# Optimization experiments

Hardware: AMD Instinct MI355X
Metric: run time of the kernel (lower is better)

The kernel has to match this reference:

```python
import jax, jax.numpy as jnp
import numpy as np

N = 50000      # nodes
E = 1600000    # edges (avg degree 32)
F_IN = 128
HID = 256
C = 40


def setup_inputs() -> dict:
    key = jax.random.key(0)
    ks = jax.random.split(key, 12)
    x = jax.random.normal(ks[0], (N, F_IN), jnp.float32)
    edge_index = jax.random.randint(ks[1], (2, E), 0, N, dtype=jnp.int32)

    def glorot(k, fan_in, fan_out):
        s = jnp.sqrt(2.0 / (fan_in + fan_out)).astype(jnp.float32)
        return jax.random.normal(k, (fan_in, fan_out), jnp.float32) * s

    return {
        "x": x,
        "edge_index": edge_index,
        "W1": glorot(ks[2], F_IN, HID), "b1": jnp.zeros((HID,), jnp.float32),
        "W2": glorot(ks[3], HID, HID),  "b2": jnp.zeros((HID,), jnp.float32),
        "W3": glorot(ks[4], HID, HID),  "b3": jnp.zeros((HID,), jnp.float32),
        "W4": glorot(ks[5], HID, C),    "b4": jnp.zeros((C,), jnp.float32),
    }


def _gcn_conv(x, W, b, src, dst, norm_e, self_norm):
    # PyG GCNConv: h = X W; out_j = sum_i norm_ij * h_i  (+ self-loop term) + b
    h = x @ W                                   # [N, F_out]
    msg = h[src] * norm_e[:, None]              # [E, F_out] gather + scale
    agg = jax.ops.segment_sum(msg, dst, num_segments=N)
    agg = agg + h * self_norm[:, None]          # self-loop contribution
    return agg + b


def reference(x, edge_index, W1, b1, W2, b2, W3, b3, W4, b4):
    src, dst = edge_index[0], edge_index[1]
    # degree on A + I (self-loops added), computed over destination nodes
    deg = jax.ops.segment_sum(jnp.ones((E,), x.dtype), dst, num_segments=N) + 1.0
    inv_sqrt = jax.lax.rsqrt(deg)               # [N]
    norm_e = inv_sqrt[src] * inv_sqrt[dst]      # [E] symmetric norm per edge
    self_norm = inv_sqrt * inv_sqrt             # [N] self-loop norm = 1/deg

    h = jax.nn.relu(_gcn_conv(x, W1, b1, src, dst, norm_e, self_norm))
    h = jax.nn.relu(_gcn_conv(h, W2, b2, src, dst, norm_e, self_norm))
    h = jax.nn.relu(_gcn_conv(h, W3, b3, src, dst, norm_e, self_norm))
    h = _gcn_conv(h, W4, b4, src, dst, norm_e, self_norm)
    return jax.nn.log_softmax(h, axis=1)
```

## Files before the change

### kernel.cpp

```cpp
#include <hip/hip_runtime.h>
#include <hip/hip_fp16.h>
#include <math.h>


typedef _Float16 f16x8 __attribute__((ext_vector_type(8)));
typedef float f32x4 __attribute__((ext_vector_type(4)));
typedef unsigned u32x4 __attribute__((ext_vector_type(4)));

#define CAP 80

#define AS1 __attribute__((address_space(1)))
#define AS3 __attribute__((address_space(3)))

__device__ __forceinline__ void dma16(const unsigned short* g,
                                      const unsigned short* ldsBase) {
    __builtin_amdgcn_global_load_lds((const AS1 void*)(size_t)g,
                                     (AS3 void*)(unsigned)(size_t)ldsBase,
                                     16, 0, 0);
}

__device__ __forceinline__ __half2 u2h2(unsigned u) {
    union { unsigned u; __half2 h; } v; v.u = u; return v.h;
}
__device__ __forceinline__ unsigned h22u(__half2 h) {
    union { unsigned u; __half2 h; } v; v.h = h; return v.u;
}
__device__ __forceinline__ float hlo(unsigned u) {
    return __half2float(__ushort_as_half((unsigned short)(u & 0xFFFFu)));
}
__device__ __forceinline__ float hhi(unsigned u) {
    return __half2float(__ushort_as_half((unsigned short)(u >> 16)));
}

__global__ __launch_bounds__(256) void count_prep_kernel(
        const int* __restrict__ dst,
        int* __restrict__ cnt, int* __restrict__ rank, int E, int nEdgeBlocks,
        const float* __restrict__ x, unsigned short* __restrict__ xb, int nx4,
        const float* __restrict__ W1, const float* __restrict__ W2,
        const float* __restrict__ W3, const float* __restrict__ W4,
        unsigned short* __restrict__ Wt1, unsigned short* __restrict__ Wt2,
        unsigned short* __restrict__ Wt3, unsigned short* __restrict__ Wt4) {
    int b = blockIdx.x;
    if (b < nEdgeBlocks) {
        int e = b * 256 + threadIdx.x;
        if (e < E) rank[e] = atomicAdd(&cnt[dst[e]], 1);
        return;
    }
    int i = (b - nEdgeBlocks) * 256 + threadIdx.x;
    if (i < nx4) {
        float4 v = reinterpret_cast<const float4*>(x)[i];
        ushort4 o;
        o.x = __half_as_ushort(__float2half_rn(v.x));
        o.y = __half_as_ushort(__float2half_rn(v.y));
        o.z = __half_as_ushort(__float2half_rn(v.z));
        o.w = __half_as_ushort(__float2half_rn(v.w));
        reinterpret_cast<ushort4*>(xb)[i] = o;
        return;
    }
    int j = i - nx4;
    if (j < 32768) {
        int k = j >> 8, n = j & 255;
        Wt1[n * 128 + k] = __half_as_ushort(__float2half_rn(W1[j]));
    } else if (j < 98304) {
        int t = j - 32768; int k = t >> 8, n = t & 255;
        Wt2[n * 256 + k] = __half_as_ushort(__float2half_rn(W2[t]));
    } else if (j < 163840) {
        int t = j - 98304; int k = t >> 8, n = t & 255;
        Wt3[n * 256 + k] = __half_as_ushort(__float2half_rn(W3[t]));
    } else if (j < 174080) {
        int t = j - 163840; int k = t / 40, n = t - k * 40;
        Wt4[n * 256 + k] = __half_as_ushort(__float2half_rn(W4[t]));
    }
}

__global__ __launch_bounds__(256) void scatter_rsq_kernel(
        const int* __restrict__ src, const int* __restrict__ dst,
        const int* __restrict__ rank, unsigned short* __restrict__ epk,
        int E, int nEdgeBlocks,
        const int* __restrict__ cnt, float* __restrict__ rsq, int N) {
    int b = blockIdx.x;
    if (b < nEdgeBlocks) {
        int e = b * 256 + threadIdx.x;
        if (e < E) {
            int d = dst[e];
            int s = src[e];
            int r = rank[e]; if (r >= CAP) r = CAP - 1;
            epk[(size_t)d * CAP + r] = (unsigned short)s;
        }
        return;
    }
    int n = (b - nEdgeBlocks) * 256 + threadIdx.x;
    if (n < N) rsq[n] = rsqrtf((float)cnt[n] + 1.0f);
}

template <int ROWB, bool WSRC, bool BIAS, bool RELU>
__global__ __launch_bounds__(256) void agg_wide_kernel(
        const unsigned short* __restrict__ G,
        const int* __restrict__ cnt,
        const unsigned short* __restrict__ epk,
        const float* __restrict__ rsq,
        const float* __restrict__ bias,
        unsigned short* __restrict__ out, int N) {
    constexpr int ROWS = ROWB / 2;
    constexpr int LPN = ROWB / 16;
    constexpr int LOG_LPN = (LPN == 32) ? 5 : 4;
    constexpr int NPW = 64 / LPN;
    int lane = threadIdx.x & 63;
    int wid = threadIdx.x >> 6;
    int sub = lane >> LOG_LPN;
    int off = lane & (LPN - 1);
    int node = blockIdx.x * (4 * NPW) + wid * NPW + sub;
    if (node >= N) return;

    const unsigned short* gb = G + off * 8;
    const unsigned short* ep = epk + (size_t)node * CAP;
    int deg = cnt[node]; if (deg > CAP) deg = CAP;

    __half2 acc[4];
    #pragma unroll
    for (int k = 0; k < 4; k++) acc[k] = u2h2(0u);

    int e = 0;
    for (; e + 7 < deg; e += 8) {
        uint4 pv = *reinterpret_cast<const uint4*>(ep + e);
        int s[8];
        s[0] = pv.x & 0xFFFFu; s[1] = pv.x >> 16;
        s[2] = pv.y & 0xFFFFu; s[3] = pv.y >> 16;
        s[4] = pv.z & 0xFFFFu; s[5] = pv.z >> 16;
        s[6] = pv.w & 0xFFFFu; s[7] = pv.w >> 16;
        uint4 v[8];
        #pragma unroll
        for (int j = 0; j < 8; j++)
            v[j] = *reinterpret_cast<const uint4*>(gb + (size_t)s[j] * ROWS);
        if (WSRC) {
            float ws[8];
            #pragma unroll
            for (int j = 0; j < 8; j++) ws[j] = rsq[s[j]];
            #pragma unroll
            for (int j = 0; j < 8; j++) {
                __half2 w2 = __half2half2(__float2half_rn(ws[j]));
                acc[0] = __hfma2(w2, u2h2(v[j].x), acc[0]);
                acc[1] = __hfma2(w2, u2h2(v[j].y), acc[1]);
                acc[2] = __hfma2(w2, u2h2(v[j].z), acc[2]);
                acc[3] = __hfma2(w2, u2h2(v[j].w), acc[3]);
            }
        } else {
            #pragma unroll
            for (int j = 0; j < 8; j++) {
                acc[0] = __hadd2(acc[0], u2h2(v[j].x));
                acc[1] = __hadd2(acc[1], u2h2(v[j].y));
                acc[2] = __hadd2(acc[2], u2h2(v[j].z));
                acc[3] = __hadd2(acc[3], u2h2(v[j].w));
            }
        }
    }
    for (; e < deg; e++) {
        int s0 = ep[e];
        uint4 v0 = *reinterpret_cast<const uint4*>(gb + (size_t)s0 * ROWS);
        if (WSRC) {
            __half2 w2 = __half2half2(__float2half_rn(rsq[s0]));
            acc[0] = __hfma2(w2, u2h2(v0.x), acc[0]);
            acc[1] = __hfma2(w2, u2h2(v0.y), acc[1]);
            acc[2] = __hfma2(w2, u2h2(v0.z), acc[2]);
            acc[3] = __hfma2(w2, u2h2(v0.w), acc[3]);
        } else {
            acc[0] = __hadd2(acc[0], u2h2(v0.x));
            acc[1] = __hadd2(acc[1], u2h2(v0.y));
            acc[2] = __hadd2(acc[2], u2h2(v0.z));
            acc[3] = __hadd2(acc[3], u2h2(v0.w));
        }
    }

    float r = rsq[node];
    uint4 sv = *reinterpret_cast<const uint4*>(gb + (size_t)node * ROWS);
    unsigned svu[4] = {sv.x, sv.y, sv.z, sv.w};
    float sw = WSRC ? r : 1.0f;
    float r2 = r * r;
    u32x4 wp;
    float4 bv0, bv1;
    if (!WSRC && BIAS) {
        bv0 = reinterpret_cast<const float4*>(bias)[off * 2];
        bv1 = reinterpret_cast<const float4*>(bias)[off * 2 + 1];
    }
    float bvf[8] = {bv0.x, bv0.y, bv0.z, bv0.w, bv1.x, bv1.y, bv1.z, bv1.w};
    #pragma unroll
    for (int k = 0; k < 4; k++) {
        float2 f = __half22float2(acc[k]);
        f.x = fmaf(sw, hlo(svu[k]), f.x);
        f.y = fmaf(sw, hhi(svu[k]), f.y);
        float ox, oy;
        if (WSRC) {
            ox = r * f.x; oy = r * f.y;
        } else {
            ox = r2 * f.x; oy = r2 * f.y;
            if (BIAS) {
                ox = fmaf(r, bvf[2 * k], ox);
                oy = fmaf(r, bvf[2 * k + 1], oy);
            }
            if (RELU) { ox = fmaxf(ox, 0.f); oy = fmaxf(oy, 0.f); }
        }
        wp[k] = h22u(__floats2half2_rn(ox, oy));
    }
    __builtin_nontemporal_store(
        wp, reinterpret_cast<u32x4*>(out + (size_t)node * ROWS + off * 8));
}

__global__ __launch_bounds__(256) void agg40_softmax_kernel(
        const unsigned short* __restrict__ G,
        const int* __restrict__ cnt,
        const unsigned short* __restrict__ epk,
        const float* __restrict__ rsq,
        const float* __restrict__ bias,
        float* __restrict__ out, int N) {
    __shared__ __align__(16) unsigned red[4][64][4];
    int lane = threadIdx.x & 63;
    int wid = threadIdx.x >> 6;
    int node = blockIdx.x * 4 + wid;
    if (node >= N) return;
    const unsigned short* ep = epk + (size_t)node * CAP;
    int deg = cnt[node]; if (deg > CAP) deg = CAP;

    int j = lane / 5;
    int c = lane - j * 5;
    __half2 a0 = u2h2(0u), a1 = u2h2(0u), a2 = u2h2(0u), a3 = u2h2(0u);
    for (int e0 = 0; e0 < deg; e0 += 12) {
        int e = e0 + j;
        unsigned m = (j < 12 && e < deg) ? 0xFFFFFFFFu : 0u;
        int ee = (e < deg) ? e : (deg - 1);
        int s = ep[ee];
        u32x4 v = *reinterpret_cast<const u32x4*>(G + (size_t)s * 40 + c * 8);
        a0 = __hadd2(a0, u2h2(v.x & m));
        a1 = __hadd2(a1, u2h2(v.y & m));
        a2 = __hadd2(a2, u2h2(v.z & m));
        a3 = __hadd2(a3, u2h2(v.w & m));
    }
    u32x4 packed;
    packed.x = h22u(a0); packed.y = h22u(a1);
    packed.z = h22u(a2); packed.w = h22u(a3);
    *reinterpret_cast<u32x4*>(&red[wid][lane][0]) = packed;
    bool act = lane < 20;
    __half2 acch = u2h2(0u);
    if (act) {
        int cc = lane >> 2;
        int w = lane & 3;
        #pragma unroll
        for (int jj = 0; jj < 12; jj++)
            acch = __hadd2(acch, u2h2(red[wid][5 * jj + cc][w]));
    }
    float lo = 0.f, hi = 0.f;
    if (act) {
        float r = rsq[node];
        unsigned sv = reinterpret_cast<const unsigned*>(G)[(size_t)node * 20 + lane];
        float2 f = __half22float2(acch);
        f.x += hlo(sv); f.y += hhi(sv);
        lo = fmaf(r, f.x, bias[2 * lane]);
        hi = fmaf(r, f.y, bias[2 * lane + 1]);
    }
    float m = act ? fmaxf(lo, hi) : -INFINITY;
    #pragma unroll
    for (int o = 32; o >= 1; o >>= 1) m = fmaxf(m, __shfl_xor(m, o, 64));
    float s = act ? (expf(lo - m) + expf(hi - m)) : 0.f;
    #pragma unroll
    for (int o = 32; o >= 1; o >>= 1) s += __shfl_xor(s, o, 64);
    float ls = logf(s);
    if (act) {
        float2 o2;
        o2.x = lo - m - ls;
        o2.y = hi - m - ls;
        *reinterpret_cast<float2*>(out + (size_t)node * 40 + 2 * lane) = o2;
    }
}

template <int BK, bool BIAS, bool RELU, bool SCALE>
__global__ __launch_bounds__(256) void gemm_f16(
        const unsigned short* __restrict__ A,
        const unsigned short* __restrict__ Bt,
        const float* __restrict__ bias,
        const float* __restrict__ rsqRow,
        unsigned short* __restrict__ Cout,
        int M, int K, int Nc) {
    constexpr int SPR = BK / 8;
    constexpr int NSTG = (128 * SPR) / 256;
    __shared__ __align__(16) unsigned short As[128 * BK];
    __shared__ __align__(16) unsigned short Bs[128 * BK];
    int tid = threadIdx.x;
    int lane = tid & 63;
    int wid = tid >> 6;
    int rowBase = blockIdx.y * 128;
    int colBase = blockIdx.x * 128;
    int waveM = (wid & 1) * 64;
    int waveN = (wid >> 1) * 64;

    f32x4 acc[4][4] = {};
    int lrow = lane & 15;
    int kgrp = (lane >> 4) * 8;

    for (int k0 = 0; k0 < K; k0 += BK) {
        #pragma unroll
        for (int c = 0; c < NSTG; c++) {
            int base16 = c * 256 + wid * 64;
            int slot = base16 + lane;
            int row = slot / SPR;
            int kp = (slot % SPR) * 8;
            int ksw = kp ^ ((row & (SPR - 1)) * 8);
            int gr = rowBase + row; if (gr >= M) gr = M - 1;
            dma16(A + (size_t)gr * K + k0 + ksw, &As[base16 * 8]);
            int gc = colBase + row; if (gc >= Nc) gc = Nc - 1;
            dma16(Bt + (size_t)gc * K + k0 + ksw, &Bs[base16 * 8]);
        }
        __syncthreads();
        #pragma unroll
        for (int kk = 0; kk < BK; kk += 32) {
            f16x8 af[4], bfr[4];
            #pragma unroll
            for (int t = 0; t < 4; t++) {
                int ra = waveM + t * 16 + lrow;
                af[t] = *reinterpret_cast<const f16x8*>(
                    &As[ra * BK + ((kk + kgrp) ^ ((ra & (SPR - 1)) * 8))]);
                int rb = waveN + t * 16 + lrow;
                bfr[t] = *reinterpret_cast<const f16x8*>(
                    &Bs[rb * BK + ((kk + kgrp) ^ ((rb & (SPR - 1)) * 8))]);
            }
            #pragma unroll
            for (int mt = 0; mt < 4; mt++)
                #pragma unroll
                for (int nt = 0; nt < 4; nt++)
                    acc[mt][nt] = __builtin_amdgcn_mfma_f32_16x16x32_f16(
                        af[mt], bfr[nt], acc[mt][nt], 0, 0, 0);
        }
        __syncthreads();
    }

    #pragma unroll
    for (int mt = 0; mt < 4; mt++) {
        #pragma unroll
        for (int r = 0; r < 4; r++) {
            int row = rowBase + waveM + mt * 16 + (lane >> 4) * 4 + r;
            if (row >= M) continue;
            float rs = SCALE ? rsqRow[row] : 1.0f;
            #pragma unroll
            for (int nt = 0; nt < 4; nt++) {
                int col = colBase + waveN + nt * 16 + (lane & 15);
                if (col >= Nc) continue;
                float v = acc[mt][nt][r];
                if (BIAS) v += bias[col];
                if (RELU) v = fmaxf(v, 0.f);
                if (SCALE) v *= rs;
                Cout[(size_t)row * Nc + col] = __half_as_ushort(__float2half_rn(v));
            }
        }
    }
}


extern "C" void kernel_launch(void* const* d_in, const int* in_sizes, int n_in,
                              void* d_out, int out_size, void* d_ws, size_t ws_size,
                              hipStream_t stream) {
    const float* x  = (const float*)d_in[0];
    const int*   ei = (const int*)d_in[1];
    const float* W1 = (const float*)d_in[2];
    const float* b1 = (const float*)d_in[3];
    const float* W2 = (const float*)d_in[4];
    const float* b2 = (const float*)d_in[5];
    const float* W3 = (const float*)d_in[6];
    const float* b3 = (const float*)d_in[7];
    const float* W4 = (const float*)d_in[8];
    const float* b4 = (const float*)d_in[9];

    const int FIN = 128, HID = 256, C = 40;
    const int N = in_sizes[0] / FIN;
    const int E = in_sizes[1] / 2;
    const int* src = ei;
    const int* dst = ei + E;

    char* w = (char*)d_ws;
    auto alloc = [&](size_t bytes) {
        char* p = w;
        w += (bytes + 255) & ~(size_t)255;
        return p;
    };
    int*   cnt    = (int*)alloc((size_t)N * 4);
    float* rsq    = (float*)alloc((size_t)N * 4);
    unsigned short* epk = (unsigned short*)alloc((size_t)N * CAP * 2);
    unsigned short* aggx = (unsigned short*)alloc((size_t)N * FIN * 2);
    unsigned short* bufA = (unsigned short*)alloc((size_t)N * HID * 2);
    unsigned short* bufB = (unsigned short*)alloc((size_t)N * HID * 2);
    unsigned short* Wt1 = (unsigned short*)alloc((size_t)FIN * HID * 2);
    unsigned short* Wt2 = (unsigned short*)alloc((size_t)HID * HID * 2);
    unsigned short* Wt3 = (unsigned short*)alloc((size_t)HID * HID * 2);
    unsigned short* Wt4 = (unsigned short*)alloc((size_t)HID * C * 2);
    unsigned short* xb = bufB;
    int* rank = (int*)aggx;

    hipMemsetAsync(cnt, 0, (size_t)N * 4, stream);

    int nx4 = N * FIN / 4;
    int nEdgeBlocks = (E + 255) / 256;
    int prepBlocks = (nx4 + 174080 + 255) / 256;
    count_prep_kernel<<<nEdgeBlocks + prepBlocks, 256, 0, stream>>>(
        dst, cnt, rank, E, nEdgeBlocks,
        x, xb, nx4, W1, W2, W3, W4, Wt1, Wt2, Wt3, Wt4);
    int rsqBlocks = (N + 255) / 256;
    scatter_rsq_kernel<<<nEdgeBlocks + rsqBlocks, 256, 0, stream>>>(
        src, dst, rank, epk, E, nEdgeBlocks, cnt, rsq, N);

    dim3 gAgg1((N + 15) / 16);
    dim3 gAggH((N + 7) / 8);
    int grp = (N + 3) / 4;
    dim3 gHID((HID + 127) / 128, (N + 127) / 128);
    dim3 gC((C + 127) / 128, (N + 127) / 128);

    agg_wide_kernel<256, true, false, false>
        <<<gAgg1, 256, 0, stream>>>(xb, cnt, epk, rsq, nullptr, aggx, N);
    gemm_f16<128, true, true, true><<<gHID, 256, 0, stream>>>(
        aggx, Wt1, b1, rsq, bufA, N, FIN, HID);
    gemm_f16<128, false, false, false><<<gHID, 256, 0, stream>>>(
        bufA, Wt2, nullptr, nullptr, bufB, N, HID, HID);
    agg_wide_kernel<512, false, true, true>
        <<<gAggH, 256, 0, stream>>>(bufB, cnt, epk, rsq, b2, bufA, N);
    gemm_f16<128, false, false, false><<<gHID, 256, 0, stream>>>(
        bufA, Wt3, nullptr, nullptr, bufB, N, HID, HID);
    agg_wide_kernel<512, false, true, true>
        <<<gAggH, 256, 0, stream>>>(bufB, cnt, epk, rsq, b3, bufA, N);
    gemm_f16<128, false, false, false><<<gC, 256, 0, stream>>>(
        bufA, Wt4, nullptr, nullptr, bufB, N, HID, C);
    agg40_softmax_kernel<<<grp, 256, 0, stream>>>(bufB, cnt, epk,
                                                  rsq, b4, (float*)d_out, N);
}
```

Baseline: 562.6 us.

## Privatize degree counters into 8 slices and vectorize edge count/scatter

Degree counting now uses 8 private counter arrays chosen by block index, which cuts atomic contention on hot destinations. Each thread handles 4 edges through int4 loads. A new small kernel prefix-sums the 8 slices into per-slice base offsets, total counts and rsqrt norms, and the scatter adds the slice base to each edge's local rank. In exchange it adds an extra kernel launch, a larger memset and 8N-sized scratch buffers.

```diff
diff --git a/kernel.cpp b/kernel.cpp
--- a/kernel.cpp
+++ b/kernel.cpp
@@ -34,16 +34,29 @@
 
 __global__ __launch_bounds__(256) void count_prep_kernel(
         const int* __restrict__ dst,
-        int* __restrict__ cnt, int* __restrict__ rank, int E, int nEdgeBlocks,
+        int* __restrict__ cnt8, int* __restrict__ rank, int E, int nEdgeBlocks,
         const float* __restrict__ x, unsigned short* __restrict__ xb, int nx4,
+        int N,
         const float* __restrict__ W1, const float* __restrict__ W2,
         const float* __restrict__ W3, const float* __restrict__ W4,
         unsigned short* __restrict__ Wt1, unsigned short* __restrict__ Wt2,
         unsigned short* __restrict__ Wt3, unsigned short* __restrict__ Wt4) {
     int b = blockIdx.x;
     if (b < nEdgeBlocks) {
-        int e = b * 256 + threadIdx.x;
-        if (e < E) rank[e] = atomicAdd(&cnt[dst[e]], 1);
+        int* cs = cnt8 + (size_t)(b & 7) * N;
+        int e0 = b * 1024 + threadIdx.x * 4;
+        if (e0 + 3 < E) {
+            int4 d4 = *reinterpret_cast<const int4*>(dst + e0);
+            int4 r4;
+            r4.x = atomicAdd(&cs[d4.x], 1);
+            r4.y = atomicAdd(&cs[d4.y], 1);
+            r4.z = atomicAdd(&cs[d4.z], 1);
+            r4.w = atomicAdd(&cs[d4.w], 1);
+            *reinterpret_cast<int4*>(rank + e0) = r4;
+        } else {
+            for (int e = e0; e < E; e++)
+                rank[e] = atomicAdd(&cs[dst[e]], 1);
+        }
         return;
     }
     int i = (b - nEdgeBlocks) * 256 + threadIdx.x;
@@ -73,24 +86,49 @@
     }
 }
 
-__global__ __launch_bounds__(256) void scatter_rsq_kernel(
+__global__ __launch_bounds__(256) void base_rsq_kernel(
+        const int* __restrict__ cnt8, int* __restrict__ sBase,
+        int* __restrict__ cnt, float* __restrict__ rsq, int N) {
+    int n = blockIdx.x * 256 + threadIdx.x;
+    if (n >= N) return;
+    int acc = 0;
+    #pragma unroll
+    for (int s = 0; s < 8; s++) {
+        int c = cnt8[(size_t)s * N + n];
+        sBase[(size_t)s * N + n] = acc;
+        acc += c;
+    }
+    cnt[n] = acc;
+    rsq[n] = rsqrtf((float)acc + 1.0f);
+}
+
+__global__ __launch_bounds__(256) void scatter_kernel(
         const int* __restrict__ src, const int* __restrict__ dst,
-        const int* __restrict__ rank, unsigned short* __restrict__ epk,
-        int E, int nEdgeBlocks,
-        const int* __restrict__ cnt, float* __restrict__ rsq, int N) {
+        const int* __restrict__ rank, const int* __restrict__ sBase,
+        unsigned short* __restrict__ epk, int E, int N) {
     int b = blockIdx.x;
-    if (b < nEdgeBlocks) {
-        int e = b * 256 + threadIdx.x;
-        if (e < E) {
+    const int* sb = sBase + (size_t)(b & 7) * N;
+    int e0 = b * 1024 + threadIdx.x * 4;
+    if (e0 + 3 < E) {
+        int4 s4 = *reinterpret_cast<const int4*>(src + e0);
+        int4 d4 = *reinterpret_cast<const int4*>(dst + e0);
+        int4 r4 = *reinterpret_cast<const int4*>(rank + e0);
+        int t;
+        t = r4.x + sb[d4.x]; if (t >= CAP) t = CAP - 1;
+        epk[(size_t)d4.x * CAP + t] = (unsigned short)s4.x;
+        t = r4.y + sb[d4.y]; if (t >= CAP) t = CAP - 1;
+        epk[(size_t)d4.y * CAP + t] = (unsigned short)s4.y;
+        t = r4.z + sb[d4.z]; if (t >= CAP) t = CAP - 1;
+        epk[(size_t)d4.z * CAP + t] = (unsigned short)s4.z;
+        t = r4.w + sb[d4.w]; if (t >= CAP) t = CAP - 1;
+        epk[(size_t)d4.w * CAP + t] = (unsigned short)s4.w;
+    } else {
+        for (int e = e0; e < E; e++) {
             int d = dst[e];
-            int s = src[e];
-            int r = rank[e]; if (r >= CAP) r = CAP - 1;
-            epk[(size_t)d * CAP + r] = (unsigned short)s;
-        }
-        return;
-    }
-    int n = (b - nEdgeBlocks) * 256 + threadIdx.x;
-    if (n < N) rsq[n] = rsqrtf((float)cnt[n] + 1.0f);
+            int t = rank[e] + sb[d]; if (t >= CAP) t = CAP - 1;
+            epk[(size_t)d * CAP + t] = (unsigned short)src[e];
+        }
+    }
 }
 
 template <int ROWB, bool WSRC, bool BIAS, bool RELU>
@@ -380,6 +418,8 @@
         return p;
     };
     int*   cnt    = (int*)alloc((size_t)N * 4);
+    int*   cnt8   = (int*)alloc((size_t)N * 8 * 4);
+    int*   sBase  = (int*)alloc((size_t)N * 8 * 4);
     float* rsq    = (float*)alloc((size_t)N * 4);
     unsigned short* epk = (unsigned short*)alloc((size_t)N * CAP * 2);
     unsigned short* aggx = (unsigned short*)alloc((size_t)N * FIN * 2);
@@ -392,17 +432,18 @@
     unsigned short* xb = bufB;
     int* rank = (int*)aggx;
 
-    hipMemsetAsync(cnt, 0, (size_t)N * 4, stream);
+    hipMemsetAsync(cnt8, 0, (size_t)N * 8 * 4, stream);
 
     int nx4 = N * FIN / 4;
-    int nEdgeBlocks = (E + 255) / 256;
+    int nEdgeBlocks = (E + 1023) / 1024;
     int prepBlocks = (nx4 + 174080 + 255) / 256;
     count_prep_kernel<<<nEdgeBlocks + prepBlocks, 256, 0, stream>>>(
-        dst, cnt, rank, E, nEdgeBlocks,
-        x, xb, nx4, W1, W2, W3, W4, Wt1, Wt2, Wt3, Wt4);
-    int rsqBlocks = (N + 255) / 256;
-    scatter_rsq_kernel<<<nEdgeBlocks + rsqBlocks, 256, 0, stream>>>(
-        src, dst, rank, epk, E, nEdgeBlocks, cnt, rsq, N);
+        dst, cnt8, rank, E, nEdgeBlocks,
+        x, xb, nx4, N, W1, W2, W3, W4, Wt1, Wt2, Wt3, Wt4);
+    base_rsq_kernel<<<(N + 255) / 256, 256, 0, stream>>>(
+        cnt8, sBase, cnt, rsq, N);
+    scatter_kernel<<<nEdgeBlocks, 256, 0, stream>>>(
+        src, dst, rank, sBase, epk, E, N);
 
     dim3 gAgg1((N + 15) / 16);
     dim3 gAggH((N + 7) / 8);
```

Result: no change. 561.7 us (-0.2%).

## Build CSR buckets with per-block LDS histograms and scan instead of global atomics

Applied to the files above, without the earlier changes.

Replaces global per-edge atomic counting and rank storage with per-block shared-memory histograms (packed 16-bit pairs), a column scan across blocks that yields per-block offsets, counts and rsq, and a second LDS pass that assigns slots during scatter. This removes contended global atomics and the rank array traffic, but adds a bcnt buffer of blocks×N/2 words and a strided scan pass. The final layer output is also stored with a 64-element row pitch so the softmax gather reads aligned 128-byte rows. Slot ordering within a node becomes block-ordered rather than atomic-ordered, which only changes fp16 summation order.

```diff
diff --git a/kernel.cpp b/kernel.cpp
--- a/kernel.cpp
+++ b/kernel.cpp
@@ -8,6 +8,8 @@
 typedef unsigned u32x4 __attribute__((ext_vector_type(4)));
 
 #define CAP 80
+#define EPB 8192
+#define MAXHDW 25024
 
 #define AS1 __attribute__((address_space(1)))
 #define AS3 __attribute__((address_space(3)))
@@ -32,21 +34,79 @@
     return __half2float(__ushort_as_half((unsigned short)(u >> 16)));
 }
 
-__global__ __launch_bounds__(256) void count_prep_kernel(
-        const int* __restrict__ dst,
-        int* __restrict__ cnt, int* __restrict__ rank, int E, int nEdgeBlocks,
+__global__ __launch_bounds__(256) void count_lds_kernel(
+        const int* __restrict__ dst, unsigned* __restrict__ bcnt,
+        int E, int HDW) {
+    __shared__ unsigned hist[MAXHDW];
+    for (int i = threadIdx.x; i < HDW; i += 256) hist[i] = 0;
+    __syncthreads();
+    int b = blockIdx.x;
+    int end = (b + 1) * EPB; if (end > E) end = E;
+    for (int e0 = b * EPB + threadIdx.x * 4; e0 < end; e0 += 1024) {
+        if (e0 + 3 < end) {
+            int4 d4 = *reinterpret_cast<const int4*>(dst + e0);
+            atomicAdd(&hist[d4.x >> 1], 1u << ((d4.x & 1) * 16));
+            atomicAdd(&hist[d4.y >> 1], 1u << ((d4.y & 1) * 16));
+            atomicAdd(&hist[d4.z >> 1], 1u << ((d4.z & 1) * 16));
+            atomicAdd(&hist[d4.w >> 1], 1u << ((d4.w & 1) * 16));
+        } else {
+            for (int e = e0; e < end && e < e0 + 4; e++) {
+                int d = dst[e];
+                atomicAdd(&hist[d >> 1], 1u << ((d & 1) * 16));
+            }
+        }
+    }
+    __syncthreads();
+    unsigned* out = bcnt + (size_t)b * HDW;
+    for (int i = threadIdx.x; i < HDW; i += 256) out[i] = hist[i];
+}
+
+__global__ __launch_bounds__(256) void scan_prep_kernel(
+        unsigned* __restrict__ bcnt, int nb, int HDW,
+        int* __restrict__ cnt, float* __restrict__ rsq, int N, int scanBlocks,
         const float* __restrict__ x, unsigned short* __restrict__ xb, int nx4,
         const float* __restrict__ W1, const float* __restrict__ W2,
         const float* __restrict__ W3, const float* __restrict__ W4,
         unsigned short* __restrict__ Wt1, unsigned short* __restrict__ Wt2,
         unsigned short* __restrict__ Wt3, unsigned short* __restrict__ Wt4) {
-    int b = blockIdx.x;
-    if (b < nEdgeBlocks) {
-        int e = b * 256 + threadIdx.x;
-        if (e < E) rank[e] = atomicAdd(&cnt[dst[e]], 1);
+    int blk = blockIdx.x;
+    if (blk < scanBlocks) {
+        int i = blk * 256 + threadIdx.x;
+        if (i >= HDW) return;
+        unsigned* bc = bcnt + i;
+        unsigned acc0 = 0, acc1 = 0;
+        int b = 0;
+        for (; b + 3 < nb; b += 4) {
+            unsigned w0 = bc[(size_t)(b + 0) * HDW];
+            unsigned w1 = bc[(size_t)(b + 1) * HDW];
+            unsigned w2 = bc[(size_t)(b + 2) * HDW];
+            unsigned w3 = bc[(size_t)(b + 3) * HDW];
+            bc[(size_t)(b + 0) * HDW] = acc0 | (acc1 << 16);
+            acc0 += w0 & 0xFFFFu; acc1 += w0 >> 16;
+            bc[(size_t)(b + 1) * HDW] = acc0 | (acc1 << 16);
+            acc0 += w1 & 0xFFFFu; acc1 += w1 >> 16;
+            bc[(size_t)(b + 2) * HDW] = acc0 | (acc1 << 16);
+            acc0 += w2 & 0xFFFFu; acc1 += w2 >> 16;
+            bc[(size_t)(b + 3) * HDW] = acc0 | (acc1 << 16);
+            acc0 += w3 & 0xFFFFu; acc1 += w3 >> 16;
+        }
+        for (; b < nb; b++) {
+            unsigned w = bc[(size_t)b * HDW];
+            bc[(size_t)b * HDW] = acc0 | (acc1 << 16);
+            acc0 += w & 0xFFFFu; acc1 += w >> 16;
+        }
+        int n0 = 2 * i, n1 = 2 * i + 1;
+        if (n0 < N) {
+            cnt[n0] = (int)acc0;
+            rsq[n0] = rsqrtf((float)acc0 + 1.0f);
+        }
+        if (n1 < N) {
+            cnt[n1] = (int)acc1;
+            rsq[n1] = rsqrtf((float)acc1 + 1.0f);
+        }
         return;
     }
-    int i = (b - nEdgeBlocks) * 256 + threadIdx.x;
+    int i = (blk - scanBlocks) * 256 + threadIdx.x;
     if (i < nx4) {
         float4 v = reinterpret_cast<const float4*>(x)[i];
         ushort4 o;
@@ -73,24 +133,40 @@
     }
 }
 
-__global__ __launch_bounds__(256) void scatter_rsq_kernel(
+__global__ __launch_bounds__(256) void scatter_lds_kernel(
         const int* __restrict__ src, const int* __restrict__ dst,
-        const int* __restrict__ rank, unsigned short* __restrict__ epk,
-        int E, int nEdgeBlocks,
-        const int* __restrict__ cnt, float* __restrict__ rsq, int N) {
+        const unsigned* __restrict__ bcnt, unsigned short* __restrict__ epk,
+        int E, int HDW) {
+    __shared__ unsigned hist[MAXHDW];
     int b = blockIdx.x;
-    if (b < nEdgeBlocks) {
-        int e = b * 256 + threadIdx.x;
-        if (e < E) {
-            int d = dst[e];
-            int s = src[e];
-            int r = rank[e]; if (r >= CAP) r = CAP - 1;
-            epk[(size_t)d * CAP + r] = (unsigned short)s;
-        }
-        return;
-    }
-    int n = (b - nEdgeBlocks) * 256 + threadIdx.x;
-    if (n < N) rsq[n] = rsqrtf((float)cnt[n] + 1.0f);
+    const unsigned* base = bcnt + (size_t)b * HDW;
+    for (int i = threadIdx.x; i < HDW; i += 256) hist[i] = base[i];
+    __syncthreads();
+    int end = (b + 1) * EPB; if (end > E) end = E;
+    for (int e0 = b * EPB + threadIdx.x * 4; e0 < end; e0 += 1024) {
+        if (e0 + 3 < end) {
+            int4 s4 = *reinterpret_cast<const int4*>(src + e0);
+            int4 d4 = *reinterpret_cast<const int4*>(dst + e0);
+            int dd[4] = {d4.x, d4.y, d4.z, d4.w};
+            int ss[4] = {s4.x, s4.y, s4.z, s4.w};
+            #pragma unroll
+            for (int j = 0; j < 4; j++) {
+                int d = dd[j];
+                unsigned old = atomicAdd(&hist[d >> 1], 1u << ((d & 1) * 16));
+                int slot = (int)((old >> ((d & 1) * 16)) & 0xFFFFu);
+                if (slot >= CAP) slot = CAP - 1;
+                epk[(size_t)d * CAP + slot] = (unsigned short)ss[j];
+            }
+        } else {
+            for (int e = e0; e < end && e < e0 + 4; e++) {
+                int d = dst[e];
+                unsigned old = atomicAdd(&hist[d >> 1], 1u << ((d & 1) * 16));
+                int slot = (int)((old >> ((d & 1) * 16)) & 0xFFFFu);
+                if (slot >= CAP) slot = CAP - 1;
+                epk[(size_t)d * CAP + slot] = (unsigned short)src[e];
+            }
+        }
+    }
 }
 
 template <int ROWB, bool WSRC, bool BIAS, bool RELU>
@@ -228,7 +304,7 @@
         unsigned m = (j < 12 && e < deg) ? 0xFFFFFFFFu : 0u;
         int ee = (e < deg) ? e : (deg - 1);
         int s = ep[ee];
-        u32x4 v = *reinterpret_cast<const u32x4*>(G + (size_t)s * 40 + c * 8);
+        u32x4 v = *reinterpret_cast<const u32x4*>(G + (size_t)s * 64 + c * 8);
         a0 = __hadd2(a0, u2h2(v.x & m));
         a1 = __hadd2(a1, u2h2(v.y & m));
         a2 = __hadd2(a2, u2h2(v.z & m));
@@ -250,7 +326,7 @@
     float lo = 0.f, hi = 0.f;
     if (act) {
         float r = rsq[node];
-        unsigned sv = reinterpret_cast<const unsigned*>(G)[(size_t)node * 20 + lane];
+        unsigned sv = reinterpret_cast<const unsigned*>(G)[(size_t)node * 32 + lane];
         float2 f = __half22float2(acch);
         f.x += hlo(sv); f.y += hhi(sv);
         lo = fmaf(r, f.x, bias[2 * lane]);
@@ -278,7 +354,7 @@
         const float* __restrict__ bias,
         const float* __restrict__ rsqRow,
         unsigned short* __restrict__ Cout,
-        int M, int K, int Nc) {
+        int M, int K, int Nc, int ldc) {
     constexpr int SPR = BK / 8;
     constexpr int NSTG = (128 * SPR) / 256;
     __shared__ __align__(16) unsigned short As[128 * BK];
@@ -346,7 +422,7 @@
                 if (BIAS) v += bias[col];
                 if (RELU) v = fmaxf(v, 0.f);
                 if (SCALE) v *= rs;
-                Cout[(size_t)row * Nc + col] = __half_as_ushort(__float2half_rn(v));
+                Cout[(size_t)row * ldc + col] = __half_as_ushort(__float2half_rn(v));
             }
         }
     }
@@ -372,6 +448,8 @@
     const int E = in_sizes[1] / 2;
     const int* src = ei;
     const int* dst = ei + E;
+    const int HDW = (N + 1) / 2;
+    const int nb = (E + EPB - 1) / EPB;
 
     char* w = (char*)d_ws;
     auto alloc = [&](size_t bytes) {
@@ -381,6 +459,7 @@
     };
     int*   cnt    = (int*)alloc((size_t)N * 4);
     float* rsq    = (float*)alloc((size_t)N * 4);
+    unsigned* bcnt = (unsigned*)alloc((size_t)nb * HDW * 4);
     unsigned short* epk = (unsigned short*)alloc((size_t)N * CAP * 2);
     unsigned short* aggx = (unsigned short*)alloc((size_t)N * FIN * 2);
     unsigned short* bufA = (unsigned short*)alloc((size_t)N * HID * 2);
@@ -390,19 +469,16 @@
     unsigned short* Wt3 = (unsigned short*)alloc((size_t)HID * HID * 2);
     unsigned short* Wt4 = (unsigned short*)alloc((size_t)HID * C * 2);
     unsigned short* xb = bufB;
-    int* rank = (int*)aggx;
-
-    hipMemsetAsync(cnt, 0, (size_t)N * 4, stream);
 
     int nx4 = N * FIN / 4;
-    int nEdgeBlocks = (E + 255) / 256;
+    int scanBlocks = (HDW + 255) / 256;
     int prepBlocks = (nx4 + 174080 + 255) / 256;
-    count_prep_kernel<<<nEdgeBlocks + prepBlocks, 256, 0, stream>>>(
-        dst, cnt, rank, E, nEdgeBlocks,
+
+    count_lds_kernel<<<nb, 256, 0, stream>>>(dst, bcnt, E, HDW);
+    scan_prep_kernel<<<scanBlocks + prepBlocks, 256, 0, stream>>>(
+        bcnt, nb, HDW, cnt, rsq, N, scanBlocks,
         x, xb, nx4, W1, W2, W3, W4, Wt1, Wt2, Wt3, Wt4);
-    int rsqBlocks = (N + 255) / 256;
-    scatter_rsq_kernel<<<nEdgeBlocks + rsqBlocks, 256, 0, stream>>>(
-        src, dst, rank, epk, E, nEdgeBlocks, cnt, rsq, N);
+    scatter_lds_kernel<<<nb, 256, 0, stream>>>(src, dst, bcnt, epk, E, HDW);
 
     dim3 gAgg1((N + 15) / 16);
     dim3 gAggH((N + 7) / 8);
@@ -413,17 +489,17 @@
     agg_wide_kernel<256, true, false, false>
         <<<gAgg1, 256, 0, stream>>>(xb, cnt, epk, rsq, nullptr, aggx, N);
     gemm_f16<128, true, true, true><<<gHID, 256, 0, stream>>>(
-        aggx, Wt1, b1, rsq, bufA, N, FIN, HID);
+        aggx, Wt1, b1, rsq, bufA, N, FIN, HID, HID);
     gemm_f16<128, false, false, false><<<gHID, 256, 0, stream>>>(
-        bufA, Wt2, nullptr, nullptr, bufB, N, HID, HID);
+        bufA, Wt2, nullptr, nullptr, bufB, N, HID, HID, HID);
     agg_wide_kernel<512, false, true, true>
         <<<gAggH, 256, 0, stream>>>(bufB, cnt, epk, rsq, b2, bufA, N);
     gemm_f16<128, false, false, false><<<gHID, 256, 0, stream>>>(
-        bufA, Wt3, nullptr, nullptr, bufB, N, HID, HID);
+        bufA, Wt3, nullptr, nullptr, bufB, N, HID, HID, HID);
     agg_wide_kernel<512, false, true, true>
         <<<gAggH, 256, 0, stream>>>(bufB, cnt, epk, rsq, b3, bufA, N);
     gemm_f16<128, false, false, false><<<gC, 256, 0, stream>>>(
-        bufA, Wt4, nullptr, nullptr, bufB, N, HID, C);
+        bufA, Wt4, nullptr, nullptr, bufB, N, HID, C, 64);
     agg40_softmax_kernel<<<grp, 256, 0, stream>>>(bufB, cnt, epk,
                                                   rsq, b4, (float*)d_out, N);
 }
```

After: 525.6 us (median of 2 runs). 1.07x faster.
